# Kernel tuning notes

Hardware: AMD Instinct MI355X
Metric: run time of the kernel (lower is better)

## Reference

```python
import jax, jax.numpy as jnp
import numpy as np

N, TI, TO1 = 8, 200, 51
V, E, H, J, L = 1024, 512, 512, 512, 3
ENC_D = 512


def setup_inputs() -> dict:
    key = jax.random.key(0)
    ks = jax.random.split(key, 11)
    s = lambda k, shape, sc: jax.random.normal(k, shape, jnp.float32) * sc
    return {
        "enc_out": s(ks[0], (N, TI, ENC_D), 1.0),
        "tgt_pad": jax.random.randint(ks[1], (N, TO1), 0, V),
        "embed": s(ks[2], (V, E), 0.02),          # nn.Embedding weight
        "w_ih": s(ks[3], (L, 4 * H, E), 0.04),    # LSTM input-hidden (gate order i,f,g,o)
        "w_hh": s(ks[4], (L, 4 * H, H), 0.04),    # LSTM hidden-hidden
        "b_ih": s(ks[5], (L, 4 * H), 0.04),
        "b_hh": s(ks[6], (L, 4 * H), 0.04),
        "enc_w": s(ks[7], (J, ENC_D), 0.04),      # enc_proj (no bias)
        "dec_w": s(ks[8], (J, H), 0.04),          # dec_proj weight
        "dec_b": s(ks[9], (J,), 0.04),            # dec_proj bias
        "out_w": s(ks[10], (V, J), 0.04),         # output (no bias)
    }


def lstm_layer(x, wih, whh, bih, bhh):
    # x: [N, T, E] -> [N, T, H]; PyTorch LSTM gate order i, f, g, o
    n = x.shape[0]
    h0 = jnp.zeros((n, whh.shape[1]), x.dtype)
    c0 = jnp.zeros_like(h0)
    gin = jnp.einsum('nte,ge->ntg', x, wih) + bih + bhh  # precompute input contributions

    def step(carry, g_t):
        h, c = carry
        g = g_t + h @ whh.T
        i, f, gg, o = jnp.split(g, 4, axis=-1)
        c = jax.nn.sigmoid(f) * c + jax.nn.sigmoid(i) * jnp.tanh(gg)
        h = jax.nn.sigmoid(o) * jnp.tanh(c)
        return (h, c), h

    _, hs = jax.lax.scan(step, (h0, c0), jnp.swapaxes(gin, 0, 1))
    return jnp.swapaxes(hs, 0, 1)


def reference(enc_out, tgt_pad, embed, w_ih, w_hh, b_ih, b_hh, enc_w, dec_w, dec_b, out_w):
    # embedding lookup
    x = embed[tgt_pad]                                   # [N, To+1, E]
    # 3-layer unidirectional LSTM
    for l in range(w_ih.shape[0]):
        x = lstm_layer(x, w_ih[l], w_hh[l], b_ih[l], b_hh[l])
    # projections
    enc_p = jnp.einsum('ntd,jd->ntj', enc_out, enc_w)    # [N, Ti, J]
    dec_p = jnp.einsum('nud,jd->nuj', x, dec_w) + dec_b  # [N, To+1, J]
    # joint: broadcast add -> tanh -> output linear (no bias)
    add = enc_p[:, :, None, :] + dec_p[:, None, :, :]    # [N, Ti, To+1, J]
    return jnp.einsum('ntuj,vj->ntuv', jnp.tanh(add), out_w)  # [N, Ti, To+1, V]
```

## Files before the change

### kernel.cpp

```cpp
#include <hip/hip_runtime.h>
#include <cstdint>
#include <cstddef>

typedef __attribute__((ext_vector_type(4))) float f32x4;
typedef __attribute__((ext_vector_type(8))) short bf16x8;
typedef __attribute__((ext_vector_type(8))) unsigned short u16x8;
typedef __attribute__((ext_vector_type(4))) float float4v;
typedef __attribute__((ext_vector_type(2))) unsigned long long u64x2;
typedef unsigned long long ull;

#define NB   8
#define TIN  200
#define TO1  51
#define VSZ  1024
#define HSZ  512
static constexpr int MJOINT = NB * TIN * TO1;
static constexpr int MROWS  = TO1 * NB;

static constexpr size_t B_ENCBF = 0;
static constexpr size_t B_ENCW  = B_ENCBF + 1664ull*512*2;
static constexpr size_t B_DECW  = B_ENCW  + 512ull*512*2;
static constexpr size_t B_OUTW  = B_DECW  + 512ull*512*2;
static constexpr size_t B_WIH   = B_OUTW  + 1024ull*512*2;
static constexpr size_t B_WHH   = B_WIH   + 3ull*2048*512*2;
static constexpr size_t B_XTR   = B_WHH   + 3ull*2048*512*2;
static constexpr size_t B_BSUM  = B_XTR   + 4ull*408*512*2;
static constexpr size_t B_FLAGS = B_BSUM  + 3ull*2048*4;
static constexpr size_t B_ENCP  = B_FLAGS + 8192;
static constexpr size_t B_DECP  = B_ENCP  + 1664ull*512*4;
static constexpr size_t B_ABUF  = B_DECP  + 512ull*512*4;

__device__ __forceinline__ unsigned short f2bf(float f) {
  union { float f; unsigned u; } v; v.f = f;
  unsigned r = v.u + 0x7FFFu + ((v.u >> 16) & 1u);
  return (unsigned short)(r >> 16);
}
__device__ __forceinline__ float fast_tanh(float x) {
  float t = __expf(2.0f * x);
  return 1.0f - 2.0f / (t + 1.0f);
}
__device__ __forceinline__ float fast_sig(float x) {
  return 1.0f / (1.0f + __expf(-x));
}
__device__ __forceinline__ void gll16(const void* g, void* l) {
  __builtin_amdgcn_global_load_lds(
      (const __attribute__((address_space(1))) unsigned int*)g,
      (__attribute__((address_space(3))) unsigned int*)l, 16, 0, 0);
}
__device__ __forceinline__ void cvt8(const float* s, unsigned short* d) {
  const float4v* sp = (const float4v*)s;
  float4v x = sp[0], y = sp[1];
  u16x8 o;
  o[0]=f2bf(x[0]); o[1]=f2bf(x[1]); o[2]=f2bf(x[2]); o[3]=f2bf(x[3]);
  o[4]=f2bf(y[0]); o[5]=f2bf(y[1]); o[6]=f2bf(y[2]); o[7]=f2bf(y[3]);
  *(u16x8*)d = o;
}
#define ALOAD(P)     __hip_atomic_load((P), __ATOMIC_RELAXED, __HIP_MEMORY_SCOPE_AGENT)
#define ASTORE(P, V) __hip_atomic_store((P), (V), __ATOMIC_RELAXED, __HIP_MEMORY_SCOPE_AGENT)

static constexpr int N_ENC  = 102400;
static constexpr int N_ENCW = 32768;
static constexpr int N_DECW = 32768;
static constexpr int N_OUTW = 65536;
static constexpr int N_WIH  = 393216;
static constexpr int P0 = N_ENC, P1 = P0+N_ENCW, P2 = P1+N_DECW, P3 = P2+N_OUTW,
                     P4 = P3+N_WIH;

__global__ __launch_bounds__(256) void prep_all(const float* __restrict__ enc,
                                                const float* __restrict__ encw,
                                                const float* __restrict__ decw,
                                                const float* __restrict__ outw,
                                                const float* __restrict__ wih,
                                                const float* __restrict__ whh,
                                                const float* __restrict__ emb,
                                                const int* __restrict__ tgt,
                                                const float* __restrict__ bih,
                                                const float* __restrict__ bhh,
                                                unsigned short* __restrict__ d_enc,
                                                unsigned short* __restrict__ d_encw,
                                                unsigned short* __restrict__ d_decw,
                                                unsigned short* __restrict__ d_outw,
                                                unsigned short* __restrict__ d_wih,
                                                unsigned short* __restrict__ d_whh,
                                                unsigned short* __restrict__ x0,
                                                float* __restrict__ bsum,
                                                int* __restrict__ flags) {
  if (blockIdx.x == 0 && threadIdx.x < 97) flags[threadIdx.x * 16] = 0;
  if (blockIdx.x >= 4086) {
    int i = (blockIdx.x - 4086) * 2048 + threadIdx.x * 8;
#pragma unroll
    for (int k = 0; k < 8; ++k) bsum[i + k] = bih[i + k] + bhh[i + k];
    return;
  }
  if (blockIdx.x >= 3984) {
    int idx = (blockIdx.x - 3984) * 256 + threadIdx.x;
    if (idx >= MROWS * 64) return;
    int m = idx >> 6, kc = (idx & 63) * 8;
    int t = m >> 3, n = m & 7;
    int v = tgt[n * TO1 + t];
    cvt8(emb + (size_t)v * 512 + kc, x0 + (size_t)m * 512 + kc);
    return;
  }
  int i = blockIdx.x * 256 + threadIdx.x;
  const float* s; unsigned short* d; int rel;
  if      (i < P0) { s = enc;  d = d_enc;  rel = i; }
  else if (i < P1) { s = encw; d = d_encw; rel = i - P0; }
  else if (i < P2) { s = decw; d = d_decw; rel = i - P1; }
  else if (i < P3) { s = outw; d = d_outw; rel = i - P2; }
  else if (i < P4) { s = wih;  d = d_wih;  rel = i - P3; }
  else             { s = whh;  d = d_whh;  rel = i - P4; }
  cvt8(s + (size_t)rel * 8, d + (size_t)rel * 8);
}

__global__ __launch_bounds__(512, 2) void gemm256(const unsigned short* __restrict__ A,
                                                  const unsigned short* __restrict__ B,
                                                  float* __restrict__ C,
                                                  int M, int N, int K) {
  __shared__ __align__(16) unsigned short lds[2][2][8192];
  const int tid = threadIdx.x;
  const int wave = tid >> 6, lane = tid & 63;
  const int lr = lane & 15, lg = lane >> 4;
  const int wr = (wave >> 2) * 128;
  const int wc = (wave & 3) * 64;

  const int nwg = gridDim.x * gridDim.y;
  const int id = blockIdx.y * gridDim.x + blockIdx.x;
  const int q = nwg >> 3, r = nwg & 7, xcd = id & 7, rest = id >> 3;
  const int nid = (xcd < r ? xcd * (q + 1) : r * (q + 1) + (xcd - r) * q) + rest;
  const size_t n0 = (size_t)(nid % gridDim.x) * 256;
  const size_t m0 = (size_t)(nid / gridDim.x) * 256;

  f32x4 acc[8][4];
#pragma unroll
  for (int i = 0; i < 8; ++i)
#pragma unroll
    for (int j = 0; j < 4; ++j) acc[i][j] = (f32x4){0.f, 0.f, 0.f, 0.f};

#define STG(bf, kt)                                                                    \
  do {                                                                                 \
    _Pragma("unroll") for (int u = 0; u < 2; ++u) {                                    \
      const int idx = u * 512 + tid;                                                   \
      const int row_ = idx >> 2;                                                       \
      const int ch = (idx & 3) ^ (row_ & 3);                                           \
      gll16(A + (m0 + row_) * (size_t)K + (kt) + ch * 8,                               \
            &lds[bf][0][(u * 512 + wave * 64) * 8]);                                   \
    }                                                                                  \
    _Pragma("unroll") for (int u = 0; u < 2; ++u) {                                    \
      const int idx = u * 512 + tid;                                                   \
      const int row_ = idx >> 2;                                                       \
      const int ch = (idx & 3) ^ (row_ & 3);                                           \
      gll16(B + (n0 + row_) * (size_t)K + (kt) + ch * 8,                               \
            &lds[bf][1][(u * 512 + wave * 64) * 8]);                                   \
    }                                                                                  \
  } while (0)

  const int nt = K >> 5;
  int cur = 0;
  STG(0, 0);
  for (int t = 0; t < nt; ++t) {
    if (t + 1 < nt) {
      STG(cur ^ 1, (t + 1) * 32);
      asm volatile("s_waitcnt vmcnt(4)" ::: "memory");
    } else {
      asm volatile("s_waitcnt vmcnt(0)" ::: "memory");
    }
    __builtin_amdgcn_s_barrier();
    const unsigned short* As_ = lds[cur][0];
    const unsigned short* Bs_ = lds[cur][1];
    bf16x8 b[4];
#pragma unroll
    for (int j = 0; j < 4; ++j) {
      const int rb = wc + j * 16 + lr;
      b[j] = *(const bf16x8*)&Bs_[rb * 32 + ((lg ^ (rb & 3)) << 3)];
    }
    __builtin_amdgcn_s_setprio(1);
#pragma unroll
    for (int i = 0; i < 8; ++i) {
      const int ra = wr + i * 16 + lr;
      bf16x8 a0 = *(const bf16x8*)&As_[ra * 32 + ((lg ^ (ra & 3)) << 3)];
#pragma unroll
      for (int j = 0; j < 4; ++j)
        acc[i][j] = __builtin_amdgcn_mfma_f32_16x16x32_bf16(a0, b[j], acc[i][j], 0, 0, 0);
    }
    __builtin_amdgcn_s_setprio(0);
    __builtin_amdgcn_s_barrier();
    cur ^= 1;
  }
#undef STG

#pragma unroll
  for (int i = 0; i < 8; ++i) {
#pragma unroll
    for (int q2 = 0; q2 < 4; ++q2) {
      const long m = (long)m0 + wr + i * 16 + lg * 4 + q2;
      if (m < M) {
        float* crow = C + (size_t)m * N + n0 + wc;
#pragma unroll
        for (int j = 0; j < 4; ++j) crow[j * 16 + lr] = acc[i][j][q2];
      }
    }
  }
}

__global__ __launch_bounds__(256) void mega_kernel(const unsigned short* __restrict__ wih,
                                                   const unsigned short* __restrict__ whh,
                                                   const float* __restrict__ bsum,
                                                   unsigned short* __restrict__ xtr,
                                                   int* __restrict__ flags,
                                                   const unsigned short* __restrict__ eA,
                                                   const unsigned short* __restrict__ eB,
                                                   float* __restrict__ eC,
                                                   const unsigned short* __restrict__ decw,
                                                   const float* __restrict__ dec_b,
                                                   const float* __restrict__ encp,
                                                   unsigned short* __restrict__ abuf) {
  __shared__ __align__(16) unsigned short w_s[64 * 1024];
  __shared__ __align__(16) unsigned short x_s[8 * 512];
  __shared__ __align__(16) unsigned short h_s[8 * 512];
  __shared__ float gates_s[4][8][16];

  const int tid = threadIdx.x;
  const int wave = tid >> 6, lane = tid & 63;
  const int lr = lane & 15, lg = lane >> 4;
  const int r7 = lr & 7;

  if (blockIdx.x >= 148) {
    const int wkr = blockIdx.x - 148;
    unsigned short* h3_s = x_s;
    float* decp_row = (float*)w_s;
    const unsigned short* xtr3 = xtr + 3ull * MROWS * 512;
#pragma unroll 1
    for (int k = 0; k < 4; ++k) {
      const int j = wkr + 102 * k;
      const int u = j >> 3;
      const int p = j & 7;
      if (wave == 0) {
        for (;;) {
          bool ok = true;
          if (lane < 32) ok = ALOAD(&flags[(64 + lane) * 16]) >= u + 1;
          else if (lane == 32) ok = ALOAD(&flags[96 * 16]) >= 52;
          if (__all(ok)) break;
          __builtin_amdgcn_s_sleep(1);
        }
      }
      __syncthreads();
      {
        const int sr2 = tid >> 5, sc2 = tid & 31;
        const ull* ph = (const ull*)(xtr3 + ((size_t)u * 8 + sr2) * 512);
#pragma unroll
        for (int k2 = 0; k2 < 2; ++k2) {
          const int c_ = sc2 + k2 * 32;
          ull v0 = ALOAD(ph + c_ * 2), v1 = ALOAD(ph + c_ * 2 + 1);
          *(u64x2*)&h3_s[sr2 * 512 + ((c_ ^ sr2) << 3)] = (u64x2){v0, v1};
        }
      }
      __syncthreads();
      {
        const int colbase = wave * 128;
#pragma unroll
        for (int ct = 0; ct < 8; ++ct) {
          f32x4 acc = (f32x4){0.f, 0.f, 0.f, 0.f};
          const int col = colbase + ct * 16 + lr;
#pragma unroll
          for (int c16 = 0; c16 < 16; ++c16) {
            const int cc = c16 * 4 + lg;
            bf16x8 av = *(const bf16x8*)&h3_s[r7 * 512 + ((cc ^ r7) << 3)];
            bf16x8 bv = *(const bf16x8*)&decw[(size_t)col * 512 + cc * 8];
            acc = __builtin_amdgcn_mfma_f32_16x16x32_bf16(av, bv, acc, 0, 0, 0);
          }
#pragma unroll
          for (int q2 = 0; q2 < 4; ++q2)
            if (lg * 4 + q2 == p) decp_row[col] = acc[q2] + dec_b[col];
        }
      }
      __syncthreads();
      {
        const int tr = tid >> 6;
        const int colc = (lane) * 8;
        for (int pass = 0; pass < 50; ++pass) {
          const int nt = p * 200 + pass * 4 + tr;
          const float4v* pe = (const float4v*)(encp + (size_t)nt * 512 + colc);
          float4v e0 = pe[0], e1 = pe[1];
          u16x8 o;
#pragma unroll
          for (int w2 = 0; w2 < 4; ++w2) {
            o[w2]     = f2bf(fast_tanh(e0[w2] + decp_row[colc + w2]));
            o[4 + w2] = f2bf(fast_tanh(e1[w2] + decp_row[colc + 4 + w2]));
          }
          *(u16x8*)&abuf[((size_t)nt * TO1 + u) * 512 + colc] = o;
        }
      }
      __syncthreads();
    }
    return;
  }

  if (blockIdx.x >= 96) {
    unsigned short* eld = w_s;
    const int g = blockIdx.x - 96;
    const int wm = (wave >> 1) * 64, wn = (wave & 1) * 64;
    const int xsl = (lg ^ (lr & 3)) << 3;
    const int nwg = 52;
    const int q = nwg >> 3, r = nwg & 7, xcd = g & 7, rest = g >> 3;
    const int nid = (xcd < r ? xcd * (q + 1) : r * (q + 1) + (xcd - r) * q) + rest;
    const size_t n0 = (size_t)(nid & 3) * 128;
    const size_t m0 = (size_t)(nid >> 2) * 128;

    f32x4 acc[4][4];
#pragma unroll
    for (int i = 0; i < 4; ++i)
#pragma unroll
      for (int j = 0; j < 4; ++j) acc[i][j] = (f32x4){0.f, 0.f, 0.f, 0.f};

#define ESTG(bf, kt)                                                                   \
    do {                                                                               \
      _Pragma("unroll") for (int u = 0; u < 2; ++u) {                                  \
        const int s = u * 256 + tid;                                                   \
        const int row_ = s >> 2;                                                       \
        const int ch = (s & 3) ^ (row_ & 3);                                           \
        gll16(eA + (m0 + row_) * 512 + (kt) + ch * 8,                                  \
              &eld[(bf) * 8192 + (u * 256 + wave * 64) * 8]);                          \
      }                                                                                \
      _Pragma("unroll") for (int u = 0; u < 2; ++u) {                                  \
        const int s = u * 256 + tid;                                                   \
        const int row_ = s >> 2;                                                       \
        const int ch = (s & 3) ^ (row_ & 3);                                           \
        gll16(eB + (n0 + row_) * 512 + (kt) + ch * 8,                                  \
              &eld[(bf) * 8192 + 4096 + (u * 256 + wave * 64) * 8]);                   \
      }                                                                                \
    } while (0)

    int cur = 0;
    ESTG(0, 0);
    for (int t = 0; t < 16; ++t) {
      if (t + 1 < 16) {
        ESTG(cur ^ 1, (t + 1) * 32);
        asm volatile("s_waitcnt vmcnt(4)" ::: "memory");
      } else {
        asm volatile("s_waitcnt vmcnt(0)" ::: "memory");
      }
      __builtin_amdgcn_s_barrier();
      const unsigned short* As_ = eld + cur * 8192;
      const unsigned short* Bs_ = As_ + 4096;
      bf16x8 a[4], b[4];
#pragma unroll
      for (int i = 0; i < 4; ++i) a[i] = *(const bf16x8*)&As_[(wm + i * 16 + lr) * 32 + xsl];
#pragma unroll
      for (int j = 0; j < 4; ++j) b[j] = *(const bf16x8*)&Bs_[(wn + j * 16 + lr) * 32 + xsl];
      __builtin_amdgcn_s_setprio(1);
#pragma unroll
      for (int i = 0; i < 4; ++i)
#pragma unroll
        for (int j = 0; j < 4; ++j)
          acc[i][j] = __builtin_amdgcn_mfma_f32_16x16x32_bf16(a[i], b[j], acc[i][j], 0, 0, 0);
      __builtin_amdgcn_s_setprio(0);
      __builtin_amdgcn_s_barrier();
      cur ^= 1;
    }
#undef ESTG

    const int rq = lg * 4;
#pragma unroll
    for (int j = 0; j < 4; ++j) {
      const int col = (int)n0 + wn + j * 16 + lr;
#pragma unroll
      for (int i = 0; i < 4; ++i) {
#pragma unroll
        for (int q2 = 0; q2 < 4; ++q2) {
          const long m = (long)m0 + wm + i * 16 + rq + q2;
          ASTORE(&eC[(size_t)m * 512 + col], acc[i][j][q2]);
        }
      }
    }
    asm volatile("s_waitcnt vmcnt(0)" ::: "memory");
    __syncthreads();
    if (tid == 0)
      __hip_atomic_fetch_add(&flags[96 * 16], 1, __ATOMIC_RELAXED, __HIP_MEMORY_SCOPE_AGENT);
    return;
  }

  const int l = blockIdx.x >> 5;
  const int b32 = blockIdx.x & 31;
  const int hid0 = b32 << 4;
  const int rw = wave * 16 + lr;

  {
    const int rl = tid >> 2;
    const int qt = tid & 3;
    const size_t R = (size_t)l * 2048 + (size_t)(rl >> 4) * 512 + hid0 + (rl & 15);
    const unsigned short* s0 = wih + R * 512;
    const unsigned short* s1 = whh + R * 512;
#pragma unroll
    for (int i = 0; i < 32; ++i) {
      int c = qt * 32 + i;
      bf16x8 wv = (c < 64) ? *(const bf16x8*)&s0[c * 8] : *(const bf16x8*)&s1[(c - 64) * 8];
      *(bf16x8*)&w_s[rl * 1024 + ((c ^ (rl & 7)) << 3)] = wv;
    }
  }
  const float bias = bsum[(size_t)l * 2048 + (size_t)wave * 512 + hid0 + lr];

  const unsigned short* xin = xtr + (size_t)l * MROWS * 512;
  unsigned short* xout = xtr + (size_t)(l + 1) * MROWS * 512;
  float c_reg = 0.f;
  const int srow = tid >> 5;
  const int sc = tid & 31;
  __syncthreads();

  f32x4 ax0, ax1;

  if (l > 0) {
    if (wave == 0) {
      for (;;) {
        bool ok_ = true;
        if (lane < 32)
          ok_ = ALOAD(&flags[((l - 1) * 32 + lane) * 16]) >= 1;
        if (__all(ok_)) break;
        __builtin_amdgcn_s_sleep(1);
      }
    }
  }
  __syncthreads();
  {
    const ull* px = (const ull*)(xin + (size_t)srow * 512);
#pragma unroll
    for (int k_ = 0; k_ < 2; ++k_) {
      const int c_ = sc + k_ * 32;
      ull v0 = ALOAD(px + c_ * 2), v1 = ALOAD(px + c_ * 2 + 1);
      *(u64x2*)&x_s[srow * 512 + ((c_ ^ srow) << 3)] = (u64x2){v0, v1};
    }
  }
  __syncthreads();
  ax0 = (f32x4){0.f, 0.f, 0.f, 0.f};
  ax1 = (f32x4){0.f, 0.f, 0.f, 0.f};
#pragma unroll
  for (int c16 = 0; c16 < 16; ++c16) {
    const int cc = c16 * 4 + lg;
    bf16x8 av = *(const bf16x8*)&x_s[r7 * 512 + ((cc ^ r7) << 3)];
    bf16x8 bv = *(const bf16x8*)&w_s[rw * 1024 + ((cc ^ r7) << 3)];
    if (c16 & 1) ax1 = __builtin_amdgcn_mfma_f32_16x16x32_bf16(av, bv, ax1, 0, 0, 0);
    else         ax0 = __builtin_amdgcn_mfma_f32_16x16x32_bf16(av, bv, ax0, 0, 0, 0);
  }

  for (int t = 0; t < TO1; ++t) {
    const bool doH = (t > 0);
    const bool doX = (t + 1 < TO1);
    if (doH || (doX && l > 0)) {
      if (wave == 0) {
        for (;;) {
          bool ok_ = true;
          if (lane < 32) {
            if (doH) ok_ = ALOAD(&flags[(l * 32 + lane) * 16]) >= t;
          } else {
            if (doX && l > 0)
              ok_ = ALOAD(&flags[((l - 1) * 32 + (lane - 32)) * 16]) >= t + 2;
          }
          if (__all(ok_)) break;
          __builtin_amdgcn_s_sleep(1);
        }
      }
    }
    __syncthreads();

    {
      ull vh[4], vx[4];
      const ull* ph = (const ull*)(xout + ((size_t)(t - 1) * 8 + srow) * 512);
      const ull* px = (const ull*)(xin + ((size_t)(t + 1) * 8 + srow) * 512);
#pragma unroll
      for (int k_ = 0; k_ < 2; ++k_) {
        const int c_ = sc + k_ * 32;
        if (doH) { vh[2 * k_] = ALOAD(ph + c_ * 2); vh[2 * k_ + 1] = ALOAD(ph + c_ * 2 + 1); }
        if (doX) { vx[2 * k_] = ALOAD(px + c_ * 2); vx[2 * k_ + 1] = ALOAD(px + c_ * 2 + 1); }
      }
#pragma unroll
      for (int k_ = 0; k_ < 2; ++k_) {
        const int c_ = sc + k_ * 32;
        if (doH) *(u64x2*)&h_s[srow * 512 + ((c_ ^ srow) << 3)] = (u64x2){vh[2 * k_], vh[2 * k_ + 1]};
        if (doX) *(u64x2*)&x_s[srow * 512 + ((c_ ^ srow) << 3)] = (u64x2){vx[2 * k_], vx[2 * k_ + 1]};
      }
    }
    __syncthreads();

    f32x4 acc0 = ax0, acc1 = ax1;
    if (doH) {
#pragma unroll
      for (int c16 = 0; c16 < 16; ++c16) {
        const int cc = c16 * 4 + lg;
        bf16x8 av = *(const bf16x8*)&h_s[r7 * 512 + ((cc ^ r7) << 3)];
        bf16x8 bv = *(const bf16x8*)&w_s[rw * 1024 + (((64 + cc) ^ r7) << 3)];
        if (c16 & 1) acc1 = __builtin_amdgcn_mfma_f32_16x16x32_bf16(av, bv, acc1, 0, 0, 0);
        else         acc0 = __builtin_amdgcn_mfma_f32_16x16x32_bf16(av, bv, acc0, 0, 0, 0);
      }
    }

    {
      f32x4 g = acc0 + acc1;
      const int nb4 = lg * 4;
#pragma unroll
      for (int q2 = 0; q2 < 4; ++q2) {
        int n = nb4 + q2;
        if (n < 8) gates_s[wave][n][lr] = g[q2] + bias;
      }
    }
    __syncthreads();
    if (tid < 128) {
      const int n = tid >> 4, j = tid & 15;
      float gi = gates_s[0][n][j], gf = gates_s[1][n][j];
      float gg = gates_s[2][n][j], go = gates_s[3][n][j];
      c_reg = fast_sig(gf) * c_reg + fast_sig(gi) * fast_tanh(gg);
      float ht = fast_sig(go) * fast_tanh(c_reg);
      float htn = __shfl_down(ht, 1);
      if (!(j & 1)) {
        unsigned pk = (unsigned)f2bf(ht) | ((unsigned)f2bf(htn) << 16);
        ASTORE((unsigned*)(xout + ((size_t)t * 8 + n) * 512 + hid0 + j), pk);
      }
    }
    asm volatile("s_waitcnt vmcnt(0)" ::: "memory");
    __syncthreads();
    if (tid == 0)
      ASTORE(&flags[(l * 32 + b32) * 16], t + 1);

    if (doX) {
      ax0 = (f32x4){0.f, 0.f, 0.f, 0.f};
      ax1 = (f32x4){0.f, 0.f, 0.f, 0.f};
#pragma unroll
      for (int c16 = 0; c16 < 16; ++c16) {
        const int cc = c16 * 4 + lg;
        bf16x8 av = *(const bf16x8*)&x_s[r7 * 512 + ((cc ^ r7) << 3)];
        bf16x8 bv = *(const bf16x8*)&w_s[rw * 1024 + ((cc ^ r7) << 3)];
        if (c16 & 1) ax1 = __builtin_amdgcn_mfma_f32_16x16x32_bf16(av, bv, ax1, 0, 0, 0);
        else         ax0 = __builtin_amdgcn_mfma_f32_16x16x32_bf16(av, bv, ax0, 0, 0, 0);
      }
    }
  }
}

extern "C" void kernel_launch(void* const* d_in, const int* in_sizes, int n_in,
                              void* d_out, int out_size, void* d_ws, size_t ws_size,
                              hipStream_t stream) {
  (void)in_sizes; (void)n_in; (void)out_size; (void)ws_size;
  const float* enc_out = (const float*)d_in[0];
  const int*   tgt     = (const int*)d_in[1];
  const float* embed   = (const float*)d_in[2];
  const float* w_ih    = (const float*)d_in[3];
  const float* w_hh    = (const float*)d_in[4];
  const float* b_ih    = (const float*)d_in[5];
  const float* b_hh    = (const float*)d_in[6];
  const float* enc_w   = (const float*)d_in[7];
  const float* dec_w   = (const float*)d_in[8];
  const float* dec_b   = (const float*)d_in[9];
  const float* out_w   = (const float*)d_in[10];

  char* ws = (char*)d_ws;
  unsigned short* enc_bf  = (unsigned short*)(ws + B_ENCBF);
  unsigned short* encw_bf = (unsigned short*)(ws + B_ENCW);
  unsigned short* decw_bf = (unsigned short*)(ws + B_DECW);
  unsigned short* outw_bf = (unsigned short*)(ws + B_OUTW);
  unsigned short* wih_bf  = (unsigned short*)(ws + B_WIH);
  unsigned short* whh_bf  = (unsigned short*)(ws + B_WHH);
  unsigned short* xtr     = (unsigned short*)(ws + B_XTR);
  float* bsum  = (float*)(ws + B_BSUM);
  int*   flags = (int*)(ws + B_FLAGS);
  float* encp  = (float*)(ws + B_ENCP);
  unsigned short* abuf = (unsigned short*)(ws + B_ABUF);
  float* Cout  = (float*)d_out;

  prep_all<<<4089, 256, 0, stream>>>(enc_out, enc_w, dec_w, out_w, w_ih, w_hh,
                                     embed, tgt, b_ih, b_hh,
                                     enc_bf, encw_bf, decw_bf, outw_bf, wih_bf, whh_bf,
                                     xtr, bsum, flags);

  mega_kernel<<<250, 256, 0, stream>>>(wih_bf, whh_bf, bsum, xtr, flags,
                                       enc_bf, encw_bf, encp,
                                       decw_bf, dec_b, encp, abuf);

  gemm256<<<dim3(4, 319), 512, 0, stream>>>(abuf, outw_bf, Cout, MJOINT, VSZ, 512);
}
```

Baseline: 338.8 us.

## Widen GEMM K-tile to 64 and interleave staged loads with MFMA quarters

The 256x256 bf16 GEMM now stages K=64 per tile instead of 32, using an 8-chunk XOR swizzle and doubling LDS to 128 KB, which drops the two-blocks-per-CU launch bound. Each tile's global-to-LDS loads for the next stage are split into four pieces and issued between four compute sub-phases, each with its own barrier. The aim is half as many outer iterations and barrier waits, with load issue spread across compute to hide latency. The loop count is now hardcoded to 8, so it assumes K=512, and occupancy falls to one block per CU.

After: 325.7 us, median of 2. 1.04x faster.

```diff
diff --git a/kernel.cpp b/kernel.cpp
--- a/kernel.cpp
+++ b/kernel.cpp
@@ -112,11 +112,11 @@
   cvt8(s + (size_t)rel * 8, d + (size_t)rel * 8);
 }
 
-__global__ __launch_bounds__(512, 2) void gemm256(const unsigned short* __restrict__ A,
-                                                  const unsigned short* __restrict__ B,
-                                                  float* __restrict__ C,
-                                                  int M, int N, int K) {
-  __shared__ __align__(16) unsigned short lds[2][2][8192];
+__global__ __launch_bounds__(512) void gemm256(const unsigned short* __restrict__ A,
+                                               const unsigned short* __restrict__ B,
+                                               float* __restrict__ C,
+                                               int M, int N, int K) {
+  __shared__ __align__(16) unsigned short lds[2][2][16384];
   const int tid = threadIdx.x;
   const int wave = tid >> 6, lane = tid & 63;
   const int lr = lane & 15, lg = lane >> 4;
@@ -136,57 +136,66 @@
 #pragma unroll
     for (int j = 0; j < 4; ++j) acc[i][j] = (f32x4){0.f, 0.f, 0.f, 0.f};
 
-#define STG(bf, kt)                                                                    \
-  do {                                                                                 \
-    _Pragma("unroll") for (int u = 0; u < 2; ++u) {                                    \
-      const int idx = u * 512 + tid;                                                   \
-      const int row_ = idx >> 2;                                                       \
-      const int ch = (idx & 3) ^ (row_ & 3);                                           \
-      gll16(A + (m0 + row_) * (size_t)K + (kt) + ch * 8,                               \
-            &lds[bf][0][(u * 512 + wave * 64) * 8]);                                   \
-    }                                                                                  \
-    _Pragma("unroll") for (int u = 0; u < 2; ++u) {                                    \
-      const int idx = u * 512 + tid;                                                   \
-      const int row_ = idx >> 2;                                                       \
-      const int ch = (idx & 3) ^ (row_ & 3);                                           \
-      gll16(B + (n0 + row_) * (size_t)K + (kt) + ch * 8,                               \
-            &lds[bf][1][(u * 512 + wave * 64) * 8]);                                   \
-    }                                                                                  \
+#define STGH(bf, kt, h)                                                                 \
+  do {                                                                                  \
+    const unsigned short* SRC_ = ((h) < 2) ? A : B;                                     \
+    const size_t base_ = ((h) < 2) ? m0 : n0;                                           \
+    _Pragma("unroll") for (int u = 0; u < 2; ++u) {                                     \
+      const int idx2 = u * 512 + tid;                                                   \
+      const int rloc = (idx2 >> 3) + (((h) & 1) << 7);                                  \
+      const int ch = (idx2 & 7) ^ (rloc & 7);                                           \
+      gll16(SRC_ + (base_ + rloc) * (size_t)K + (kt) + ch * 8,                          \
+            &lds[bf][(h) >> 1][((((h) & 1) << 10) + u * 512 + wave * 64) * 8]);         \
+    }                                                                                   \
   } while (0)
 
-  const int nt = K >> 5;
+  STGH(0, 0, 0); STGH(0, 0, 1); STGH(0, 0, 2); STGH(0, 0, 3);
+
   int cur = 0;
-  STG(0, 0);
-  for (int t = 0; t < nt; ++t) {
-    if (t + 1 < nt) {
-      STG(cur ^ 1, (t + 1) * 32);
-      asm volatile("s_waitcnt vmcnt(4)" ::: "memory");
-    } else {
-      asm volatile("s_waitcnt vmcnt(0)" ::: "memory");
-    }
-    __builtin_amdgcn_s_barrier();
+  for (int t = 0; t < 8; ++t) {
+    const int nxt = cur ^ 1;
     const unsigned short* As_ = lds[cur][0];
     const unsigned short* Bs_ = lds[cur][1];
-    bf16x8 b[4];
-#pragma unroll
-    for (int j = 0; j < 4; ++j) {
-      const int rb = wc + j * 16 + lr;
-      b[j] = *(const bf16x8*)&Bs_[rb * 32 + ((lg ^ (rb & 3)) << 3)];
-    }
-    __builtin_amdgcn_s_setprio(1);
-#pragma unroll
-    for (int i = 0; i < 8; ++i) {
-      const int ra = wr + i * 16 + lr;
-      bf16x8 a0 = *(const bf16x8*)&As_[ra * 32 + ((lg ^ (ra & 3)) << 3)];
-#pragma unroll
-      for (int j = 0; j < 4; ++j)
-        acc[i][j] = __builtin_amdgcn_mfma_f32_16x16x32_bf16(a0, b[j], acc[i][j], 0, 0, 0);
-    }
-    __builtin_amdgcn_s_setprio(0);
-    __builtin_amdgcn_s_barrier();
-    cur ^= 1;
-  }
-#undef STG
+    bf16x8 b[4][2];
+#pragma unroll
+    for (int p = 0; p < 4; ++p) {
+      if (t + 1 < 8) STGH(nxt, (t + 1) * 64, p);
+      if (p == 0) {
+        if (t + 1 < 8) asm volatile("s_waitcnt vmcnt(2)" ::: "memory");
+        else           asm volatile("s_waitcnt vmcnt(0)" ::: "memory");
+        __builtin_amdgcn_s_barrier();
+#pragma unroll
+        for (int j = 0; j < 4; ++j) {
+          const int rb = wc + j * 16 + lr;
+          const int sw = rb & 7;
+          b[j][0] = *(const bf16x8*)&Bs_[rb * 64 + ((lg ^ sw) << 3)];
+          b[j][1] = *(const bf16x8*)&Bs_[rb * 64 + (((4 + lg) ^ sw) << 3)];
+        }
+      }
+      bf16x8 a[2][2];
+#pragma unroll
+      for (int i2 = 0; i2 < 2; ++i2) {
+        const int ra = wr + (p * 2 + i2) * 16 + lr;
+        const int swa = ra & 7;
+        a[i2][0] = *(const bf16x8*)&As_[ra * 64 + ((lg ^ swa) << 3)];
+        a[i2][1] = *(const bf16x8*)&As_[ra * 64 + (((4 + lg) ^ swa) << 3)];
+      }
+      __builtin_amdgcn_s_setprio(1);
+#pragma unroll
+      for (int i2 = 0; i2 < 2; ++i2) {
+        const int i = p * 2 + i2;
+#pragma unroll
+        for (int j = 0; j < 4; ++j) {
+          acc[i][j] = __builtin_amdgcn_mfma_f32_16x16x32_bf16(a[i2][0], b[j][0], acc[i][j], 0, 0, 0);
+          acc[i][j] = __builtin_amdgcn_mfma_f32_16x16x32_bf16(a[i2][1], b[j][1], acc[i][j], 0, 0, 0);
+        }
+      }
+      __builtin_amdgcn_s_setprio(0);
+      __builtin_amdgcn_s_barrier();
+    }
+    cur = nxt;
+  }
+#undef STGH
 
 #pragma unroll
   for (int i = 0; i < 8; ++i) {
```
